# Kernel optimization log

Hardware: AMD Instinct MI355X
Metric: run time of the kernel (lower is better)

Reference implementation:

```python
import jax, jax.numpy as jnp
import numpy as np

EMBED_DIM = 1024
NUM_HEADS = 16
HEAD_DIM = EMBED_DIM // NUM_HEADS


def setup_inputs() -> dict:
    key = jax.random.key(0)
    ks = jax.random.split(key, 11)
    B, N, C = 2, 2048, EMBED_DIM
    s = 1.0 / np.sqrt(C)
    return {
        "query": jax.random.normal(ks[0], (B, N, C), jnp.float32),
        "key": jax.random.normal(ks[1], (B, N, C), jnp.float32),
        "value": jax.random.normal(ks[2], (B, N, C), jnp.float32),
        # torch nn.Linear weights: [out_features, in_features]
        "Wq": jax.random.normal(ks[3], (C, C), jnp.float32) * s,
        "bq": jnp.zeros((C,), jnp.float32),
        "Wk": jax.random.normal(ks[4], (C, C), jnp.float32) * s,
        "bk": jnp.zeros((C,), jnp.float32),
        "Wv": jax.random.normal(ks[5], (C, C), jnp.float32) * s,
        "bv": jnp.zeros((C,), jnp.float32),
        "Wo": jax.random.normal(ks[6], (C, C), jnp.float32) * s,
        "bo": jnp.zeros((C,), jnp.float32),
    }


def reference(query, key, value, Wq, bq, Wk, bk, Wv, bv, Wo, bo):
    B, N, C = query.shape
    H, D = NUM_HEADS, HEAD_DIM
    # projections (torch Linear: x @ W.T + b)
    q = query @ Wq.T + bq
    k = key @ Wk.T + bk
    v = value @ Wv.T + bv
    # [B, N, C] -> [B, H, N, D]
    q = q.reshape(B, N, H, D).transpose(0, 2, 1, 3)
    k = k.reshape(B, N, H, D).transpose(0, 2, 1, 3)
    v = v.reshape(B, N, H, D).transpose(0, 2, 1, 3)
    # scores: [B, H, N, N]
    scores = jnp.einsum("bhqd,bhkd->bhqk", q, k) / jnp.sqrt(jnp.asarray(D, q.dtype))
    attn = jax.nn.softmax(scores, axis=-1)
    # attend: [B, H, N, D] -> [B, N, C]
    out = jnp.einsum("bhqk,bhkd->bhqd", attn, v)
    out = out.transpose(0, 2, 1, 3).reshape(B, N, C)
    return out @ Wo.T + bo
```

## Files before the change

kernel.cpp:

```cpp
#include <hip/hip_runtime.h>
#include <hip/hip_bf16.h>
#include <cstdint>

typedef short bf16x8 __attribute__((ext_vector_type(8)));
typedef float f32x4 __attribute__((ext_vector_type(4)));
typedef float f32x16 __attribute__((ext_vector_type(16)));
typedef uint32_t u32x4v __attribute__((ext_vector_type(4)));
typedef unsigned short u16;

#define BATCH 2
#define NTOK 2048
#define CDIM 1024
#define NHEAD 16
#define DHEAD 64
#define MROWS 4096
#define KDIM 1024
#define KVB 128
#define NT (NTOK / KVB)

__device__ __forceinline__ u16 f2bf(float x) {
    uint32_t b = __float_as_uint(x);
    uint32_t r = (b + 0x7fffu + ((b >> 16) & 1u)) >> 16;
    return (u16)r;
}

__device__ __forceinline__ uint32_t packbf2(float lo, float hi) {
    float2 f; f.x = lo; f.y = hi;
    __hip_bfloat162 h = __float22bfloat162_rn(f);
    uint32_t r;
    __builtin_memcpy(&r, &h, 4);
    return r;
}

__device__ __forceinline__ void gload_lds16(const void* g, void* l) {
    __builtin_amdgcn_global_load_lds((const __attribute__((address_space(1))) void*)g,
                                     (__attribute__((address_space(3))) void*)l,
                                     16, 0, 0);
}

__global__ __launch_bounds__(256) void cast_kernel(
    const float* __restrict__ q, const float* __restrict__ k, const float* __restrict__ v,
    const float* __restrict__ wq, const float* __restrict__ wk, const float* __restrict__ wv,
    const float* __restrict__ wo, u16* __restrict__ dst) {
    const size_t TOT = 16u << 20;
    size_t i0 = ((size_t)blockIdx.x * 256 + threadIdx.x) * 4;
    size_t stride = (size_t)gridDim.x * 256 * 4;
    for (size_t i = i0; i < TOT; i += stride) {
        const float* src;
        size_t off = i;
        if (i < (4u << 20))        { src = q;  }
        else if (i < (8u << 20))   { src = k;  off = i - (4u << 20); }
        else if (i < (12u << 20))  { src = v;  off = i - (8u << 20); }
        else if (i < (13u << 20))  { src = wq; off = i - (12u << 20); }
        else if (i < (14u << 20))  { src = wk; off = i - (13u << 20); }
        else if (i < (15u << 20))  { src = wv; off = i - (14u << 20); }
        else                       { src = wo; off = i - (15u << 20); }
        float4 f = *(const float4*)(src + off);
        uint2 packed;
        packed.x = packbf2(f.x, f.y);
        packed.y = packbf2(f.z, f.w);
        *(uint2*)(dst + i) = packed;
    }
}

__global__ __launch_bounds__(256, 3) void gemm_qkv(
    const u16* __restrict__ Xq, const u16* __restrict__ Xk, const u16* __restrict__ Xv,
    const u16* __restrict__ Wq, const u16* __restrict__ Wk, const u16* __restrict__ Wv,
    const float* __restrict__ bq, const float* __restrict__ bk, const float* __restrict__ bv,
    u16* __restrict__ Qo, u16* __restrict__ Ko, u16* __restrict__ Vo) {
    __shared__ u16 sA[128 * 32];
    __shared__ u16 sB[128 * 32];
    const int tid = threadIdx.x;
    const int lane = tid & 63;
    const int wave = tid >> 6;
    const int z = blockIdx.z;
    const u16* A  = (z == 0) ? Xq : (z == 1) ? Xk : Xv;
    const u16* Bw = (z == 0) ? Wq : (z == 1) ? Wk : Wv;
    const float* bias = (z == 0) ? bq : (z == 1) ? bk : bv;
    u16* Out = (z == 0) ? Qo : (z == 1) ? Ko : Vo;
    const float scale = (z == 0) ? 0.125f * 1.44269504088896f : 1.0f;

    const int m0 = blockIdx.x * 128, n0 = blockIdx.y * 128;
    const int wm = (wave >> 1) * 64, wn = (wave & 1) * 64;
    f32x4 acc[4][4] = {};
    const int rsel = lane & 15;
    const int ksel = (lane >> 4) * 8;

    for (int k0 = 0; k0 < KDIM; k0 += 32) {
#pragma unroll
        for (int u = 0; u < 2; ++u) {
            int c = tid + u * 256;
            int row = c >> 2, cin = c & 3;
            gload_lds16(A + (size_t)(m0 + row) * KDIM + k0 + cin * 8, &sA[c * 8]);
            gload_lds16(Bw + (size_t)(n0 + row) * KDIM + k0 + cin * 8, &sB[c * 8]);
        }
        __syncthreads();
        bf16x8 af[4], bfr[4];
#pragma unroll
        for (int i = 0; i < 4; ++i)
            af[i] = *(const bf16x8*)&sA[(wm + i * 16 + rsel) * 32 + ksel];
#pragma unroll
        for (int j = 0; j < 4; ++j)
            bfr[j] = *(const bf16x8*)&sB[(wn + j * 16 + rsel) * 32 + ksel];
#pragma unroll
        for (int i = 0; i < 4; ++i)
#pragma unroll
            for (int j = 0; j < 4; ++j)
                acc[i][j] = __builtin_amdgcn_mfma_f32_16x16x32_bf16(af[i], bfr[j], acc[i][j], 0, 0, 0);
        __syncthreads();
    }

    if (z != 2) {
#pragma unroll
        for (int i = 0; i < 4; ++i) {
            int mbase = m0 + wm + i * 16 + (lane >> 4) * 4;
#pragma unroll
            for (int j = 0; j < 4; ++j) {
                int n = n0 + wn + j * 16 + (lane & 15);
                float bv2 = bias[n];
                int h = n >> 6, d = n & 63;
#pragma unroll
                for (int r = 0; r < 4; ++r) {
                    int m = mbase + r;
                    int b = m >> 11, tok = m & 2047;
                    Out[(((size_t)(b * NHEAD + h)) * NTOK + tok) * DHEAD + d] =
                        f2bf((acc[i][j][r] + bv2) * scale);
                }
            }
        }
    } else {
#pragma unroll
        for (int i = 0; i < 4; ++i) {
            int mbase = m0 + wm + i * 16 + (lane >> 4) * 4;
            int b = mbase >> 11, tok = mbase & 2047;
#pragma unroll
            for (int j = 0; j < 4; ++j) {
                int n = n0 + wn + j * 16 + (lane & 15);
                float bv2 = bias[n];
                int h = n >> 6, d = n & 63;
                uint2 st;
                st.x = packbf2(acc[i][j][0] + bv2, acc[i][j][1] + bv2);
                st.y = packbf2(acc[i][j][2] + bv2, acc[i][j][3] + bv2);
                *(uint2*)&Out[(((size_t)(b * NHEAD + h)) * DHEAD + d) * NTOK + tok] = st;
            }
        }
    }
}

__global__ __launch_bounds__(256, 3) void gemm_out(
    const u16* __restrict__ A,
    const u16* __restrict__ Bw,
    const float* __restrict__ bias,
    float* __restrict__ Out,
    int M, int N, int K) {
    __shared__ u16 sA[128 * 32];
    __shared__ u16 sB[128 * 32];
    const int tid = threadIdx.x;
    const int lane = tid & 63;
    const int wave = tid >> 6;
    const int m0 = blockIdx.x * 128, n0 = blockIdx.y * 128;
    const int wm = (wave >> 1) * 64, wn = (wave & 1) * 64;
    f32x4 acc[4][4] = {};
    const int rsel = lane & 15;
    const int ksel = (lane >> 4) * 8;

    for (int k0 = 0; k0 < K; k0 += 32) {
#pragma unroll
        for (int u = 0; u < 2; ++u) {
            int c = tid + u * 256;
            int row = c >> 2, cin = c & 3;
            gload_lds16(A + (size_t)(m0 + row) * K + k0 + cin * 8, &sA[c * 8]);
            gload_lds16(Bw + (size_t)(n0 + row) * K + k0 + cin * 8, &sB[c * 8]);
        }
        __syncthreads();
        bf16x8 af[4], bfr[4];
#pragma unroll
        for (int i = 0; i < 4; ++i)
            af[i] = *(const bf16x8*)&sA[(wm + i * 16 + rsel) * 32 + ksel];
#pragma unroll
        for (int j = 0; j < 4; ++j)
            bfr[j] = *(const bf16x8*)&sB[(wn + j * 16 + rsel) * 32 + ksel];
#pragma unroll
        for (int i = 0; i < 4; ++i)
#pragma unroll
            for (int j = 0; j < 4; ++j)
                acc[i][j] = __builtin_amdgcn_mfma_f32_16x16x32_bf16(af[i], bfr[j], acc[i][j], 0, 0, 0);
        __syncthreads();
    }

#pragma unroll
    for (int i = 0; i < 4; ++i) {
        int mbase = m0 + wm + i * 16 + (lane >> 4) * 4;
#pragma unroll
        for (int j = 0; j < 4; ++j) {
            int n = n0 + wn + j * 16 + (lane & 15);
            float bv = bias[n];
#pragma unroll
            for (int r = 0; r < 4; ++r) {
                int m = mbase + r;
                Out[(size_t)m * N + n] = acc[i][j][r] + bv;
            }
        }
    }
}

__global__ __launch_bounds__(256, 2) void attn_kernel(
    const u16* __restrict__ Qg, const u16* __restrict__ Kg, const u16* __restrict__ Vg,
    u16* __restrict__ Og) {
    __shared__ u16 Ks[2][KVB * 64];
    __shared__ u16 Vt[2][64 * KVB];
    const int tid = threadIdx.x, lane = tid & 63, wave = tid >> 6;
    const int hi = lane >> 5, lq = lane & 31;

    int flat = blockIdx.x;
    int vflat = (flat & 7) * 64 + (flat >> 3);
    int bh = vflat >> 4;
    int qtile = vflat & 15;

    const int h = bh & (NHEAD - 1), b = bh >> 4;
    const u16* Qh = Qg + (size_t)bh * NTOK * DHEAD;
    const u16* Kh = Kg + (size_t)bh * NTOK * DHEAD;
    const u16* VhT = Vg + (size_t)bh * DHEAD * NTOK;
    const int qrow0 = qtile * 128 + wave * 32;
    const int qr = qrow0 + lq;

    bf16x8 qf[4];
#pragma unroll
    for (int dk = 0; dk < 4; ++dk)
        qf[dk] = *(const bf16x8*)&Qh[(size_t)qr * DHEAD + dk * 16 + hi * 8];

    f32x16 acc0 = {}, acc1 = {};
    float lrun = 0.f;

    const int pr = ((lq >> 2) & 1) * 8 + (lq & 3) + ((lq >> 3) & 1) * 4 + (lq >> 4) * 16;

    {
#pragma unroll
        for (int u = 0; u < 4; ++u) {
            int c2 = tid + u * 256;
            int kv = c2 >> 3, gi = c2 & 7;
            gload_lds16(Kh + (size_t)kv * DHEAD + (gi ^ (kv & 7)) * 8, &Ks[0][c2 * 8]);
        }
#pragma unroll
        for (int u = 0; u < 4; ++u) {
            int c2 = tid + u * 256;
            int d = c2 >> 4, gi = c2 & 15;
            gload_lds16(VhT + (size_t)d * NTOK + (gi ^ (d & 15)) * 8, &Vt[0][c2 * 8]);
        }
    }
    __syncthreads();

    int cur = 0;
    for (int t = 0; t < NT; ++t) {
        const bool pre = (t + 1 < NT);
        if (pre) {
#pragma unroll
            for (int u = 0; u < 4; ++u) {
                int c2 = tid + u * 256;
                int kv = c2 >> 3, gi = c2 & 7;
                gload_lds16(Kh + (size_t)((t + 1) * KVB + kv) * DHEAD + (gi ^ (kv & 7)) * 8,
                            &Ks[cur ^ 1][c2 * 8]);
            }
#pragma unroll
            for (int u = 0; u < 4; ++u) {
                int c2 = tid + u * 256;
                int d = c2 >> 4, gi = c2 & 15;
                gload_lds16(VhT + (size_t)d * NTOK + (t + 1) * KVB + (gi ^ (d & 15)) * 8,
                            &Vt[cur ^ 1][c2 * 8]);
            }
        }

        const char* kb_ = (const char*)&Ks[cur][0];
        bf16x8 pf[8];
        float smv[16];
#pragma unroll
        for (int i = 0; i < 16; ++i) smv[i] = 0.f;
#pragma unroll
        for (int j = 0; j < 4; ++j) {
            f32x16 T = {};
            int kv = j * 32 + pr;
            const char* kr = kb_ + kv * 128;
            int sx = (kv & 7) << 4;
#pragma unroll
            for (int dk = 0; dk < 4; ++dk) {
                bf16x8 kf = *(const bf16x8*)(kr + ((dk * 32 + hi * 16) ^ sx));
                T = __builtin_amdgcn_mfma_f32_32x32x16_bf16(kf, qf[dk], T, 0, 0, 0);
            }
#pragma unroll
            for (int i = 0; i < 16; ++i) T[i] = __builtin_amdgcn_exp2f(T[i]);
#pragma unroll
            for (int i = 0; i < 16; ++i) smv[i] += T[i];
            u32x4v w0 = { packbf2(T[0], T[1]),  packbf2(T[2], T[3]),
                          packbf2(T[4], T[5]),  packbf2(T[6], T[7]) };
            u32x4v w1 = { packbf2(T[8], T[9]),  packbf2(T[10], T[11]),
                          packbf2(T[12], T[13]), packbf2(T[14], T[15]) };
            pf[j * 2]     = *(bf16x8*)&w0;
            pf[j * 2 + 1] = *(bf16x8*)&w1;
        }

        const char* vb_ = (const char*)&Vt[cur][0];
        __builtin_amdgcn_s_setprio(1);
#pragma unroll
        for (int db = 0; db < 2; ++db) {
            int d = db * 32 + lq;
#pragma unroll
            for (int ks = 0; ks < 8; ++ks) {
                int off = d * 256 + ((ks * 32 + hi * 16) ^ ((d & 15) << 4));
                bf16x8 vf = *(const bf16x8*)(vb_ + off);
                if (db == 0)
                    acc0 = __builtin_amdgcn_mfma_f32_32x32x16_bf16(vf, pf[ks], acc0, 0, 0, 0);
                else
                    acc1 = __builtin_amdgcn_mfma_f32_32x32x16_bf16(vf, pf[ks], acc1, 0, 0, 0);
            }
        }
        __builtin_amdgcn_s_setprio(0);

#pragma unroll
        for (int s2 = 8; s2 >= 1; s2 >>= 1)
#pragma unroll
            for (int i = 0; i < s2; ++i) smv[i] += smv[i + s2];
        lrun += smv[0] + __shfl_xor(smv[0], 32);

        __syncthreads();
        cur ^= 1;
    }

    float rinv = 1.0f / lrun;
#pragma unroll
    for (int db = 0; db < 2; ++db) {
#pragma unroll
        for (int rq = 0; rq < 4; ++rq) {
            int based = db * 32 + 8 * rq + 4 * hi;
            float o0, o1, o2, o3;
            if (db == 0) {
                o0 = acc0[rq * 4 + 0]; o1 = acc0[rq * 4 + 1];
                o2 = acc0[rq * 4 + 2]; o3 = acc0[rq * 4 + 3];
            } else {
                o0 = acc1[rq * 4 + 0]; o1 = acc1[rq * 4 + 1];
                o2 = acc1[rq * 4 + 2]; o3 = acc1[rq * 4 + 3];
            }
            uint2 st;
            st.x = packbf2(o0 * rinv, o1 * rinv);
            st.y = packbf2(o2 * rinv, o3 * rinv);
            *(uint2*)&Og[((size_t)(b * NTOK + qr)) * CDIM + h * DHEAD + based] = st;
        }
    }
}

extern "C" void kernel_launch(void* const* d_in, const int* in_sizes, int n_in,
                              void* d_out, int out_size, void* d_ws, size_t ws_size,
                              hipStream_t stream) {
    const float* q  = (const float*)d_in[0];
    const float* k  = (const float*)d_in[1];
    const float* v  = (const float*)d_in[2];
    const float* Wq = (const float*)d_in[3];
    const float* bq = (const float*)d_in[4];
    const float* Wk = (const float*)d_in[5];
    const float* bk = (const float*)d_in[6];
    const float* Wv = (const float*)d_in[7];
    const float* bv = (const float*)d_in[8];
    const float* Wo = (const float*)d_in[9];
    const float* bo = (const float*)d_in[10];

    u16* wsp = (u16*)d_ws;
    u16* Xq  = wsp;
    u16* Xk  = Xq + (4u << 20);
    u16* Xv  = Xk + (4u << 20);
    u16* Wqb = Xv + (4u << 20);
    u16* Wkb = Wqb + (1u << 20);
    u16* Wvb = Wkb + (1u << 20);
    u16* Wob = Wvb + (1u << 20);
    u16* Qb  = Wob + (1u << 20);
    u16* Kb  = Qb + (4u << 20);
    u16* Vb  = Kb + (4u << 20);
    u16* Ab  = Xq;

    cast_kernel<<<2048, 256, 0, stream>>>(q, k, v, Wq, Wk, Wv, Wo, Xq);

    gemm_qkv<<<dim3(MROWS / 128, CDIM / 128, 3), 256, 0, stream>>>(
        Xq, Xk, Xv, Wqb, Wkb, Wvb, bq, bk, bv, Qb, Kb, Vb);

    attn_kernel<<<512, 256, 0, stream>>>(Qb, Kb, Vb, Ab);

    gemm_out<<<dim3(MROWS / 128, CDIM / 128), 256, 0, stream>>>(
        Ab, Wob, bo, (float*)d_out, MROWS, CDIM, KDIM);
}
```

Measured before the change: 122.9 us.

## Fuse fp32 activation cast into QKV GEMM and compute softmax sums via MFMA

Activations are no longer cast to bf16 in a separate pass. The QKV GEMM now loads fp32 tiles straight into swizzled LDS and converts them to bf16 while building fragments, which removes a full read and write of 48MB of activations. In the attention kernel, the per-row exp sum is computed with an extra MFMA against a ones vector instead of scalar adds and a shuffle, at the cost of eight more MFMAs per tile and a 16-register accumulator. The GEMM's A tiles now take twice the LDS and global traffic per k-step, and the row sum is formed from bf16-rounded probabilities.

```diff
diff --git a/kernel.cpp b/kernel.cpp
--- a/kernel.cpp
+++ b/kernel.cpp
@@ -18,12 +18,6 @@
 #define KVB 128
 #define NT (NTOK / KVB)
 
-__device__ __forceinline__ u16 f2bf(float x) {
-    uint32_t b = __float_as_uint(x);
-    uint32_t r = (b + 0x7fffu + ((b >> 16) & 1u)) >> 16;
-    return (u16)r;
-}
-
 __device__ __forceinline__ uint32_t packbf2(float lo, float hi) {
     float2 f; f.x = lo; f.y = hi;
     __hip_bfloat162 h = __float22bfloat162_rn(f);
@@ -32,49 +26,50 @@
     return r;
 }
 
+__device__ __forceinline__ u16 f2bf(float x) {
+    return (u16)(packbf2(x, 0.f) & 0xffffu);
+}
+
 __device__ __forceinline__ void gload_lds16(const void* g, void* l) {
     __builtin_amdgcn_global_load_lds((const __attribute__((address_space(1))) void*)g,
                                      (__attribute__((address_space(3))) void*)l,
                                      16, 0, 0);
 }
 
-__global__ __launch_bounds__(256) void cast_kernel(
-    const float* __restrict__ q, const float* __restrict__ k, const float* __restrict__ v,
-    const float* __restrict__ wq, const float* __restrict__ wk, const float* __restrict__ wv,
-    const float* __restrict__ wo, u16* __restrict__ dst) {
-    const size_t TOT = 16u << 20;
+__global__ __launch_bounds__(256) void cast_w(
+    const float* __restrict__ wq, const float* __restrict__ wk,
+    const float* __restrict__ wv, const float* __restrict__ wo,
+    u16* __restrict__ dst) {
+    const size_t TOT = 4u << 20;
     size_t i0 = ((size_t)blockIdx.x * 256 + threadIdx.x) * 4;
     size_t stride = (size_t)gridDim.x * 256 * 4;
     for (size_t i = i0; i < TOT; i += stride) {
         const float* src;
         size_t off = i;
-        if (i < (4u << 20))        { src = q;  }
-        else if (i < (8u << 20))   { src = k;  off = i - (4u << 20); }
-        else if (i < (12u << 20))  { src = v;  off = i - (8u << 20); }
-        else if (i < (13u << 20))  { src = wq; off = i - (12u << 20); }
-        else if (i < (14u << 20))  { src = wk; off = i - (13u << 20); }
-        else if (i < (15u << 20))  { src = wv; off = i - (14u << 20); }
-        else                       { src = wo; off = i - (15u << 20); }
+        if (i < (1u << 20))        { src = wq; }
+        else if (i < (2u << 20))   { src = wk; off = i - (1u << 20); }
+        else if (i < (3u << 20))   { src = wv; off = i - (2u << 20); }
+        else                       { src = wo; off = i - (3u << 20); }
         float4 f = *(const float4*)(src + off);
-        uint2 packed;
-        packed.x = packbf2(f.x, f.y);
-        packed.y = packbf2(f.z, f.w);
-        *(uint2*)(dst + i) = packed;
+        uint2 p;
+        p.x = packbf2(f.x, f.y);
+        p.y = packbf2(f.z, f.w);
+        *(uint2*)(dst + i) = p;
     }
 }
 
 __global__ __launch_bounds__(256, 3) void gemm_qkv(
-    const u16* __restrict__ Xq, const u16* __restrict__ Xk, const u16* __restrict__ Xv,
+    const float* __restrict__ Xq, const float* __restrict__ Xk, const float* __restrict__ Xv,
     const u16* __restrict__ Wq, const u16* __restrict__ Wk, const u16* __restrict__ Wv,
     const float* __restrict__ bq, const float* __restrict__ bk, const float* __restrict__ bv,
     u16* __restrict__ Qo, u16* __restrict__ Ko, u16* __restrict__ Vo) {
-    __shared__ u16 sA[128 * 32];
+    __shared__ float sAf[128 * 32];
     __shared__ u16 sB[128 * 32];
     const int tid = threadIdx.x;
     const int lane = tid & 63;
     const int wave = tid >> 6;
     const int z = blockIdx.z;
-    const u16* A  = (z == 0) ? Xq : (z == 1) ? Xk : Xv;
+    const float* A = (z == 0) ? Xq : (z == 1) ? Xk : Xv;
     const u16* Bw = (z == 0) ? Wq : (z == 1) ? Wk : Wv;
     const float* bias = (z == 0) ? bq : (z == 1) ? bk : bv;
     u16* Out = (z == 0) ? Qo : (z == 1) ? Ko : Vo;
@@ -85,20 +80,34 @@
     f32x4 acc[4][4] = {};
     const int rsel = lane & 15;
     const int ksel = (lane >> 4) * 8;
+    const int cb = ksel >> 2;
 
     for (int k0 = 0; k0 < KDIM; k0 += 32) {
+#pragma unroll
+        for (int u = 0; u < 4; ++u) {
+            int c2 = tid + u * 256;
+            int row = c2 >> 3, gi = c2 & 7;
+            gload_lds16(A + (size_t)(m0 + row) * KDIM + k0 + ((gi ^ (row & 7)) << 2),
+                        &sAf[c2 * 4]);
+        }
 #pragma unroll
         for (int u = 0; u < 2; ++u) {
             int c = tid + u * 256;
             int row = c >> 2, cin = c & 3;
-            gload_lds16(A + (size_t)(m0 + row) * KDIM + k0 + cin * 8, &sA[c * 8]);
             gload_lds16(Bw + (size_t)(n0 + row) * KDIM + k0 + cin * 8, &sB[c * 8]);
         }
         __syncthreads();
         bf16x8 af[4], bfr[4];
-#pragma unroll
-        for (int i = 0; i < 4; ++i)
-            af[i] = *(const bf16x8*)&sA[(wm + i * 16 + rsel) * 32 + ksel];
+        const char* sab = (const char*)sAf;
+#pragma unroll
+        for (int i = 0; i < 4; ++i) {
+            int r = wm + i * 16 + rsel;
+            f32x4 x0 = *(const f32x4*)(sab + r * 128 + ((((cb + 0) ^ (r & 7))) << 4));
+            f32x4 x1 = *(const f32x4*)(sab + r * 128 + ((((cb + 1) ^ (r & 7))) << 4));
+            u32x4v w = { packbf2(x0[0], x0[1]), packbf2(x0[2], x0[3]),
+                         packbf2(x1[0], x1[1]), packbf2(x1[2], x1[3]) };
+            af[i] = *(bf16x8*)&w;
+        }
 #pragma unroll
         for (int j = 0; j < 4; ++j)
             bfr[j] = *(const bf16x8*)&sB[(wn + j * 16 + rsel) * 32 + ksel];
@@ -230,7 +239,9 @@
         qf[dk] = *(const bf16x8*)&Qh[(size_t)qr * DHEAD + dk * 16 + hi * 8];
 
     f32x16 acc0 = {}, acc1 = {};
-    float lrun = 0.f;
+    f32x16 lacc = {};
+    const bf16x8 ones = { (short)0x3F80, (short)0x3F80, (short)0x3F80, (short)0x3F80,
+                          (short)0x3F80, (short)0x3F80, (short)0x3F80, (short)0x3F80 };
 
     const int pr = ((lq >> 2) & 1) * 8 + (lq & 3) + ((lq >> 3) & 1) * 4 + (lq >> 4) * 16;
 
@@ -272,9 +283,6 @@
 
         const char* kb_ = (const char*)&Ks[cur][0];
         bf16x8 pf[8];
-        float smv[16];
-#pragma unroll
-        for (int i = 0; i < 16; ++i) smv[i] = 0.f;
 #pragma unroll
         for (int j = 0; j < 4; ++j) {
             f32x16 T = {};
@@ -288,8 +296,6 @@
             }
 #pragma unroll
             for (int i = 0; i < 16; ++i) T[i] = __builtin_amdgcn_exp2f(T[i]);
-#pragma unroll
-            for (int i = 0; i < 16; ++i) smv[i] += T[i];
             u32x4v w0 = { packbf2(T[0], T[1]),  packbf2(T[2], T[3]),
                           packbf2(T[4], T[5]),  packbf2(T[6], T[7]) };
             u32x4v w1 = { packbf2(T[8], T[9]),  packbf2(T[10], T[11]),
@@ -313,19 +319,16 @@
                     acc1 = __builtin_amdgcn_mfma_f32_32x32x16_bf16(vf, pf[ks], acc1, 0, 0, 0);
             }
         }
+#pragma unroll
+        for (int ks = 0; ks < 8; ++ks)
+            lacc = __builtin_amdgcn_mfma_f32_32x32x16_bf16(ones, pf[ks], lacc, 0, 0, 0);
         __builtin_amdgcn_s_setprio(0);
 
-#pragma unroll
-        for (int s2 = 8; s2 >= 1; s2 >>= 1)
-#pragma unroll
-            for (int i = 0; i < s2; ++i) smv[i] += smv[i + s2];
-        lrun += smv[0] + __shfl_xor(smv[0], 32);
-
         __syncthreads();
         cur ^= 1;
     }
 
-    float rinv = 1.0f / lrun;
+    float rinv = 1.0f / lacc[0];
 #pragma unroll
     for (int db = 0; db < 2; ++db) {
 #pragma unroll
@@ -363,22 +366,19 @@
     const float* bo = (const float*)d_in[10];
 
     u16* wsp = (u16*)d_ws;
-    u16* Xq  = wsp;
-    u16* Xk  = Xq + (4u << 20);
-    u16* Xv  = Xk + (4u << 20);
-    u16* Wqb = Xv + (4u << 20);
+    u16* Wqb = wsp;
     u16* Wkb = Wqb + (1u << 20);
     u16* Wvb = Wkb + (1u << 20);
     u16* Wob = Wvb + (1u << 20);
     u16* Qb  = Wob + (1u << 20);
     u16* Kb  = Qb + (4u << 20);
     u16* Vb  = Kb + (4u << 20);
-    u16* Ab  = Xq;
-
-    cast_kernel<<<2048, 256, 0, stream>>>(q, k, v, Wq, Wk, Wv, Wo, Xq);
+    u16* Ab  = Vb + (4u << 20);
+
+    cast_w<<<512, 256, 0, stream>>>(Wq, Wk, Wv, Wo, Wqb);
 
     gemm_qkv<<<dim3(MROWS / 128, CDIM / 128, 3), 256, 0, stream>>>(
-        Xq, Xk, Xv, Wqb, Wkb, Wvb, bq, bk, bv, Qb, Kb, Vb);
+        q, k, v, Wqb, Wkb, Wvb, bq, bk, bv, Qb, Kb, Vb);
 
     attn_kernel<<<512, 256, 0, stream>>>(Qb, Kb, Vb, Ab);
 
```

Result: no change. 124.3 us (+1.1%).

## Double GEMM K-tile to 64 with XOR-swizzled LDS layout in projection kernels

Applied to the files above, without the earlier changes.

Both projection GEMMs (QKV and output) now stage a K-slice of 64 instead of 32 per iteration, which halves the number of barrier pairs and loop trips. The 16-byte chunks in LDS are placed with an XOR swizzle on the row index so that fragment reads from the wider rows avoid bank conflicts. LDS per block doubles to 32 KB, which may limit occupancy under the 3-blocks launch bound. The scalar bf16 rounding helper is also rewritten to use the intrinsic pack path.

```diff
diff --git a/kernel.cpp b/kernel.cpp
--- a/kernel.cpp
+++ b/kernel.cpp
@@ -18,18 +18,16 @@
 #define KVB 128
 #define NT (NTOK / KVB)
 
-__device__ __forceinline__ u16 f2bf(float x) {
-    uint32_t b = __float_as_uint(x);
-    uint32_t r = (b + 0x7fffu + ((b >> 16) & 1u)) >> 16;
-    return (u16)r;
-}
-
 __device__ __forceinline__ uint32_t packbf2(float lo, float hi) {
     float2 f; f.x = lo; f.y = hi;
     __hip_bfloat162 h = __float22bfloat162_rn(f);
     uint32_t r;
     __builtin_memcpy(&r, &h, 4);
     return r;
+}
+
+__device__ __forceinline__ u16 f2bf(float x) {
+    return (u16)(packbf2(x, 0.f) & 0xffffu);
 }
 
 __device__ __forceinline__ void gload_lds16(const void* g, void* l) {
@@ -68,8 +66,8 @@
     const u16* __restrict__ Wq, const u16* __restrict__ Wk, const u16* __restrict__ Wv,
     const float* __restrict__ bq, const float* __restrict__ bk, const float* __restrict__ bv,
     u16* __restrict__ Qo, u16* __restrict__ Ko, u16* __restrict__ Vo) {
-    __shared__ u16 sA[128 * 32];
-    __shared__ u16 sB[128 * 32];
+    __shared__ u16 sA[128 * 64];
+    __shared__ u16 sB[128 * 64];
     const int tid = threadIdx.x;
     const int lane = tid & 63;
     const int wave = tid >> 6;
@@ -84,29 +82,40 @@
     const int wm = (wave >> 1) * 64, wn = (wave & 1) * 64;
     f32x4 acc[4][4] = {};
     const int rsel = lane & 15;
-    const int ksel = (lane >> 4) * 8;
-
-    for (int k0 = 0; k0 < KDIM; k0 += 32) {
-#pragma unroll
-        for (int u = 0; u < 2; ++u) {
-            int c = tid + u * 256;
-            int row = c >> 2, cin = c & 3;
-            gload_lds16(A + (size_t)(m0 + row) * KDIM + k0 + cin * 8, &sA[c * 8]);
-            gload_lds16(Bw + (size_t)(n0 + row) * KDIM + k0 + cin * 8, &sB[c * 8]);
+    const int g = lane >> 4;
+
+    for (int k0 = 0; k0 < KDIM; k0 += 64) {
+#pragma unroll
+        for (int u = 0; u < 4; ++u) {
+            int c2 = tid + u * 256;
+            int row = c2 >> 3, gi = c2 & 7;
+            int sc = (gi ^ (row & 7)) * 8;
+            gload_lds16(A + (size_t)(m0 + row) * KDIM + k0 + sc, &sA[c2 * 8]);
+            gload_lds16(Bw + (size_t)(n0 + row) * KDIM + k0 + sc, &sB[c2 * 8]);
         }
         __syncthreads();
-        bf16x8 af[4], bfr[4];
+        bf16x8 af[4][2], bfr[4][2];
+#pragma unroll
+        for (int i = 0; i < 4; ++i) {
+            int r = wm + i * 16 + rsel;
+#pragma unroll
+            for (int h2 = 0; h2 < 2; ++h2)
+                af[i][h2] = *(const bf16x8*)&sA[r * 64 + (((g + 4 * h2) ^ (r & 7)) * 8)];
+        }
+#pragma unroll
+        for (int j = 0; j < 4; ++j) {
+            int r = wn + j * 16 + rsel;
+#pragma unroll
+            for (int h2 = 0; h2 < 2; ++h2)
+                bfr[j][h2] = *(const bf16x8*)&sB[r * 64 + (((g + 4 * h2) ^ (r & 7)) * 8)];
+        }
 #pragma unroll
         for (int i = 0; i < 4; ++i)
-            af[i] = *(const bf16x8*)&sA[(wm + i * 16 + rsel) * 32 + ksel];
-#pragma unroll
-        for (int j = 0; j < 4; ++j)
-            bfr[j] = *(const bf16x8*)&sB[(wn + j * 16 + rsel) * 32 + ksel];
-#pragma unroll
-        for (int i = 0; i < 4; ++i)
 #pragma unroll
             for (int j = 0; j < 4; ++j)
-                acc[i][j] = __builtin_amdgcn_mfma_f32_16x16x32_bf16(af[i], bfr[j], acc[i][j], 0, 0, 0);
+#pragma unroll
+                for (int h2 = 0; h2 < 2; ++h2)
+                    acc[i][j] = __builtin_amdgcn_mfma_f32_16x16x32_bf16(af[i][h2], bfr[j][h2], acc[i][j], 0, 0, 0);
         __syncthreads();
     }
 
@@ -153,8 +162,8 @@
     const float* __restrict__ bias,
     float* __restrict__ Out,
     int M, int N, int K) {
-    __shared__ u16 sA[128 * 32];
-    __shared__ u16 sB[128 * 32];
+    __shared__ u16 sA[128 * 64];
+    __shared__ u16 sB[128 * 64];
     const int tid = threadIdx.x;
     const int lane = tid & 63;
     const int wave = tid >> 6;
@@ -162,29 +171,40 @@
     const int wm = (wave >> 1) * 64, wn = (wave & 1) * 64;
     f32x4 acc[4][4] = {};
     const int rsel = lane & 15;
-    const int ksel = (lane >> 4) * 8;
-
-    for (int k0 = 0; k0 < K; k0 += 32) {
-#pragma unroll
-        for (int u = 0; u < 2; ++u) {
-            int c = tid + u * 256;
-            int row = c >> 2, cin = c & 3;
-            gload_lds16(A + (size_t)(m0 + row) * K + k0 + cin * 8, &sA[c * 8]);
-            gload_lds16(Bw + (size_t)(n0 + row) * K + k0 + cin * 8, &sB[c * 8]);
+    const int g = lane >> 4;
+
+    for (int k0 = 0; k0 < K; k0 += 64) {
+#pragma unroll
+        for (int u = 0; u < 4; ++u) {
+            int c2 = tid + u * 256;
+            int row = c2 >> 3, gi = c2 & 7;
+            int sc = (gi ^ (row & 7)) * 8;
+            gload_lds16(A + (size_t)(m0 + row) * K + k0 + sc, &sA[c2 * 8]);
+            gload_lds16(Bw + (size_t)(n0 + row) * K + k0 + sc, &sB[c2 * 8]);
         }
         __syncthreads();
-        bf16x8 af[4], bfr[4];
+        bf16x8 af[4][2], bfr[4][2];
+#pragma unroll
+        for (int i = 0; i < 4; ++i) {
+            int r = wm + i * 16 + rsel;
+#pragma unroll
+            for (int h2 = 0; h2 < 2; ++h2)
+                af[i][h2] = *(const bf16x8*)&sA[r * 64 + (((g + 4 * h2) ^ (r & 7)) * 8)];
+        }
+#pragma unroll
+        for (int j = 0; j < 4; ++j) {
+            int r = wn + j * 16 + rsel;
+#pragma unroll
+            for (int h2 = 0; h2 < 2; ++h2)
+                bfr[j][h2] = *(const bf16x8*)&sB[r * 64 + (((g + 4 * h2) ^ (r & 7)) * 8)];
+        }
 #pragma unroll
         for (int i = 0; i < 4; ++i)
-            af[i] = *(const bf16x8*)&sA[(wm + i * 16 + rsel) * 32 + ksel];
-#pragma unroll
-        for (int j = 0; j < 4; ++j)
-            bfr[j] = *(const bf16x8*)&sB[(wn + j * 16 + rsel) * 32 + ksel];
-#pragma unroll
-        for (int i = 0; i < 4; ++i)
 #pragma unroll
             for (int j = 0; j < 4; ++j)
-                acc[i][j] = __builtin_amdgcn_mfma_f32_16x16x32_bf16(af[i], bfr[j], acc[i][j], 0, 0, 0);
+#pragma unroll
+                for (int h2 = 0; h2 < 2; ++h2)
+                    acc[i][j] = __builtin_amdgcn_mfma_f32_16x16x32_bf16(af[i][h2], bfr[j][h2], acc[i][j], 0, 0, 0);
         __syncthreads();
     }
 
```

Measured after the change: 118.0 us, median of 2. -4.0%, faster.
